# Kernel tuning notes

Measured on AMD Instinct MI355X. Metric: run time of the kernel, lower is better.

The kernel has to match this reference:

```python
import jax, jax.numpy as jnp
import numpy as np


def _l2norm(v, eps=1e-12):
    # torch F.normalize(dim=-1): v / clamp(||v||_2, min=eps)
    n = jnp.linalg.norm(v, axis=-1, keepdims=True)
    return v / jnp.maximum(n, eps)


def setup_inputs() -> dict:
    key = jax.random.key(0)
    ks = jax.random.split(key, 10)
    B, T, N, Ci, E, K, H = 64, 12, 1024, 64, 16, 3, 192
    O = H // 3  # subhidden size
    return {
        "x": jax.random.normal(ks[0], (B, N, Ci), jnp.float32),
        "x_window": jax.random.normal(ks[1], (B, T, N, 1), jnp.float32),
        "node_embeddings": jax.random.normal(ks[2], (N, E), jnp.float32) * 0.1,
        "ZPI": jax.random.normal(ks[3], (B, 3), jnp.float32),
        "supports_adj": jax.random.uniform(ks[4], (K, N, N), jnp.float32),
        "weights_pool": jax.random.normal(ks[5], (E, K, Ci, O), jnp.float32) * 0.1,
        "weights_pool_adj": jax.random.normal(ks[6], (E, K, Ci, O), jnp.float32) * 0.1,
        "weights_window": jax.random.normal(ks[7], (E, 1, O), jnp.float32) * 0.1,
        "bias_pool": jax.random.normal(ks[8], (E, H), jnp.float32) * 0.1,
        "T_param": jax.random.normal(ks[9], (T,), jnp.float32) * 0.1,
    }


def reference(x, x_window, node_embeddings, ZPI, supports_adj,
              weights_pool, weights_pool_adj, weights_window, bias_pool, T_param):
    N = node_embeddings.shape[0]
    K = weights_pool.shape[1]  # link_len

    # adaptive supports: softmax(relu(E E^T)) and its power series
    supports = jax.nn.softmax(jax.nn.relu(node_embeddings @ node_embeddings.T), axis=1)
    support_set = [jnp.eye(N, dtype=x.dtype), supports]
    for k in range(2, K):
        support_set.append(supports @ support_set[k - 1])
    S = jnp.stack(support_set, axis=0)  # (K, N, N)

    # per-node dynamic weights / bias
    weights = jnp.einsum('nd,dkio->nkio', node_embeddings, weights_pool)
    bias = node_embeddings @ bias_pool  # (N, H)

    # adaptive graph conv branch
    x_g = jnp.einsum('knm,bmc->bnkc', S, x)
    x_gconv = _l2norm(jnp.einsum('bnki,nkio->bno', x_g, weights))

    # static adjacency branch ('knn' repeated index = diagonal; sum over m --
    # faithful to the original torch einsum)
    weights_adj = jnp.einsum('nd,dkio->nkio', node_embeddings, weights_pool_adj)
    x_a = jnp.einsum('knn,bmc->bnkc', supports_adj, x)
    x_aconv = _l2norm(jnp.einsum('bnki,nkio->bno', x_a, weights_adj))

    # temporal window branch
    ww = jnp.einsum('nd,dio->nio', node_embeddings, weights_window)  # (N, 1, O)
    x_w = jnp.einsum('btni,nio->btno', x_window, ww)
    x_wconv = _l2norm(jnp.einsum('btno,t->bno', x_w, T_param))

    return jnp.concatenate([x_gconv, x_aconv, x_wconv], axis=-1) + bias
```

## Files before the change

kernel.cpp:

```cpp
#include <hip/hip_runtime.h>


typedef __attribute__((ext_vector_type(4))) float f32x4;
typedef __attribute__((ext_vector_type(8))) short short8;

#define DEVI static __device__ __forceinline__

DEVI short f2bf(float f) {
    unsigned int x = __builtin_bit_cast(unsigned int, f);
    x = (x + 0x7FFFu + ((x >> 16) & 1u)) >> 16;
    return (short)(unsigned short)x;
}
DEVI int swz(int row) { return ((row ^ (row >> 3)) & 7) << 3; }

DEVI f32x4 mfma16(short8 a, short8 b, f32x4 c) {
    return __builtin_amdgcn_mfma_f32_16x16x32_bf16(a, b, c, 0, 0, 0);
}

DEVI void gload16(const void* g, void* l) {
    __builtin_amdgcn_global_load_lds(
        (const __attribute__((address_space(1))) unsigned int*)g,
        (__attribute__((address_space(3))) unsigned int*)l, 16, 0, 0);
}

__global__ __launch_bounds__(256) void k_supports(const float* __restrict__ NE,
                                                  short* __restrict__ S) {
    int n = blockIdx.x, t = threadIdx.x;
    __shared__ float En[16];
    __shared__ float wsum[4];
    if (t < 16) En[t] = NE[n * 16 + t];
    __syncthreads();
    float e[4];
    float loc = 0.f;
#pragma unroll
    for (int i = 0; i < 4; ++i) {
        int m = t + 256 * i;
        const float* rp = NE + m * 16;
        float v = 0.f;
#pragma unroll
        for (int d = 0; d < 16; ++d) v += En[d] * rp[d];
        v = fmaxf(v, 0.f);
        e[i] = __expf(v);
        loc += e[i];
    }
#pragma unroll
    for (int off = 32; off; off >>= 1) loc += __shfl_xor(loc, off);
    if ((t & 63) == 0) wsum[t >> 6] = loc;
    __syncthreads();
    float inv = 1.f / (wsum[0] + wsum[1] + wsum[2] + wsum[3]);
#pragma unroll
    for (int i = 0; i < 4; ++i) S[n * 1024 + t + 256 * i] = f2bf(e[i] * inv);
}

__global__ __launch_bounds__(256) void k_small(
        const float* __restrict__ x, const float* __restrict__ xw,
        const float* __restrict__ NE, const float* __restrict__ adj,
        const float* __restrict__ wp, const float* __restrict__ wpa,
        const float* __restrict__ Tp,
        short* __restrict__ B2, short* __restrict__ A2,
        float* __restrict__ xsp, float* __restrict__ s_bn) {
    __shared__ float red[4][64];
    int bid = blockIdx.x, t = threadIdx.x;
    if (bid < 64) {
        int o = bid, j = t;
        short row[64];
        if (j < 192) {
            int kk = j >> 6, i = j & 63;
#pragma unroll
            for (int d = 0; d < 16; ++d)
                row[d] = f2bf(wp[((d * 3 + kk) * 64 + i) * 64 + o]);
#pragma unroll
            for (int k = 16; k < 64; ++k) row[k] = 0;
        } else {
            int i2 = j - 192;
#pragma unroll
            for (int k = 0; k < 16; ++k) row[k] = 0;
#pragma unroll
            for (int d = 0; d < 16; ++d)
#pragma unroll
                for (int kk = 0; kk < 3; ++kk)
                    row[16 + d * 3 + kk] = f2bf(wpa[((d * 3 + kk) * 64 + i2) * 64 + o]);
        }
        short* dst = B2 + (o * 256 + j) * 64;
#pragma unroll
        for (int q = 0; q < 8; ++q) {
            short8 v;
#pragma unroll
            for (int e2 = 0; e2 < 8; ++e2) v[e2] = row[q * 8 + e2];
            *reinterpret_cast<short8*>(dst + q * 8) = v;
        }
    } else if (bid < 320) {
        int idx = bid - 64, b = idx >> 2, mq = idx & 3;
        int c = t & 63, q2 = t >> 6;
        int m0 = mq * 256 + q2 * 64;
        float s = 0.f;
        for (int mm = 0; mm < 64; ++mm) s += x[(b * 1024 + m0 + mm) * 64 + c];
        red[q2][c] = s;
        __syncthreads();
        if (t < 64) xsp[(b * 4 + mq) * 64 + t] = red[0][t] + red[1][t] + red[2][t] + red[3][t];
    } else if (bid < 336) {
        int idx = bid - 320;
        float tp[12];
#pragma unroll
        for (int i = 0; i < 12; ++i) tp[i] = Tp[i];
        for (int bb = 0; bb < 4; ++bb) {
            int b = idx * 4 + bb;
#pragma unroll
            for (int j2 = 0; j2 < 4; ++j2) {
                int nn = t + 256 * j2;
                float s = 0.f;
#pragma unroll
                for (int tt = 0; tt < 12; ++tt) s += xw[(b * 12 + tt) * 1024 + nn] * tp[tt];
                s_bn[b * 1024 + nn] = s;
            }
        }
    } else {
        int n = (bid - 336) * 256 + t;
        float En[16];
#pragma unroll
        for (int d = 0; d < 16; ++d) En[d] = NE[n * 16 + d];
        float dg[3];
#pragma unroll
        for (int k = 0; k < 3; ++k) dg[k] = adj[k * 1024 * 1024 + n * 1024 + n];
        short row[64];
#pragma unroll
        for (int d = 0; d < 16; ++d) row[d] = f2bf(En[d]);
#pragma unroll
        for (int d = 0; d < 16; ++d)
#pragma unroll
            for (int k = 0; k < 3; ++k) row[16 + d * 3 + k] = f2bf(En[d] * dg[k]);
        short* dst = A2 + n * 64;
#pragma unroll
        for (int q = 0; q < 8; ++q) {
            short8 v;
#pragma unroll
            for (int e2 = 0; e2 < 8; ++e2) v[e2] = row[q * 8 + e2];
            *reinterpret_cast<short8*>(dst + q * 8) = v;
        }
    }
}

__global__ __launch_bounds__(256) void k_prep(const float* __restrict__ x,
                                              const short* __restrict__ S,
                                              const float* __restrict__ xsp,
                                              short* __restrict__ ST,
                                              short* __restrict__ XT,
                                              short* __restrict__ xs_bf) {
    __shared__ __align__(16) short Tbuf[64 * 128];
    int bid = blockIdx.x, t = threadIdx.x;
    if (bid < 512) {
        int b = bid >> 3, m0 = (bid & 7) * 128;
        const float* xp = x + ((size_t)b * 1024 + m0) * 64;
#pragma unroll
        for (int p = 0; p < 8; ++p) {
            int idx = t + 256 * p;
            int r = idx >> 4, c4 = (idx & 15) * 4;
            float4 v = *reinterpret_cast<const float4*>(&xp[r * 64 + c4]);
            Tbuf[(c4 + 0) * 128 + r] = f2bf(v.x);
            Tbuf[(c4 + 1) * 128 + r] = f2bf(v.y);
            Tbuf[(c4 + 2) * 128 + r] = f2bf(v.z);
            Tbuf[(c4 + 3) * 128 + r] = f2bf(v.w);
        }
        __syncthreads();
#pragma unroll
        for (int p = 0; p < 4; ++p) {
            int idx = t + 256 * p;
            int c = idx >> 4, q = idx & 15;
            *reinterpret_cast<short8*>(&XT[((size_t)b * 64 + c) * 1024 + m0 + q * 8]) =
                *reinterpret_cast<const short8*>(&Tbuf[c * 128 + q * 8]);
        }
    } else if (bid < 768) {
        int idx = bid - 512, bi = idx >> 4, bj = idx & 15;
        int c8 = (t & 7) * 8;
#pragma unroll
        for (int p = 0; p < 2; ++p) {
            int r = (t >> 3) + 32 * p;
            short8 v = *reinterpret_cast<const short8*>(
                &S[(size_t)(bi * 64 + r) * 1024 + bj * 64 + c8]);
#pragma unroll
            for (int e = 0; e < 8; ++e) Tbuf[(c8 + e) * 64 + r] = v[e];
        }
        __syncthreads();
#pragma unroll
        for (int p = 0; p < 2; ++p) {
            int r = (t >> 3) + 32 * p;
            *reinterpret_cast<short8*>(&ST[(size_t)(bj * 64 + r) * 1024 + bi * 64 + c8]) =
                *reinterpret_cast<const short8*>(&Tbuf[r * 64 + c8]);
        }
    } else {
        int j = (bid - 768) * 256 + t;
        int b = j >> 6, c = j & 63;
        float s = xsp[(b * 4 + 0) * 64 + c] + xsp[(b * 4 + 1) * 64 + c] +
                  xsp[(b * 4 + 2) * 64 + c] + xsp[(b * 4 + 3) * 64 + c];
        xs_bf[j] = f2bf(s);
    }
}

DEVI void mm_tile(const short* __restrict__ A, const short* __restrict__ Bt,
                  short* __restrict__ C, int ldC) {
    __shared__ __align__(16) short As[128 * 64];
    __shared__ __align__(16) short Bs[128 * 64];
    int t = threadIdx.x, wid = t >> 6, lane = t & 63;
    int rsub = lane >> 3, csub = (lane & 7) * 8;
    int wm = wid & 1, wn = wid >> 1;
    int lr = lane & 15, lg = lane >> 4;
    f32x4 acc[4][4] = {};
    for (int kt = 0; kt < 16; ++kt) {
#pragma unroll
        for (int q = 0; q < 4; ++q) {
            int row = q * 32 + wid * 8;
            gload16(A + (size_t)(row + rsub) * 1024 + kt * 64 + csub, As + row * 64);
            gload16(Bt + (size_t)(row + rsub) * 1024 + kt * 64 + csub, Bs + row * 64);
        }
        __syncthreads();
#pragma unroll
        for (int ks = 0; ks < 2; ++ks) {
            int kk = ks * 32 + lg * 8;
            short8 af[4], bfv[4];
#pragma unroll
            for (int i = 0; i < 4; ++i)
                af[i] = *reinterpret_cast<const short8*>(&As[(wm * 64 + i * 16 + lr) * 64 + kk]);
#pragma unroll
            for (int i = 0; i < 4; ++i)
                bfv[i] = *reinterpret_cast<const short8*>(&Bs[(wn * 64 + i * 16 + lr) * 64 + kk]);
#pragma unroll
            for (int mf = 0; mf < 4; ++mf)
#pragma unroll
                for (int nf = 0; nf < 4; ++nf)
                    acc[mf][nf] = mfma16(af[mf], bfv[nf], acc[mf][nf]);
        }
        __syncthreads();
    }
#pragma unroll
    for (int mf = 0; mf < 4; ++mf)
#pragma unroll
        for (int nf = 0; nf < 4; ++nf)
#pragma unroll
            for (int r = 0; r < 4; ++r) {
                int g = wm * 64 + mf * 16 + lg * 4 + r;
                int j = wn * 64 + nf * 16 + lr;
                C[(size_t)g * ldC + j] = f2bf(acc[mf][nf][r]);
            }
}

__global__ __launch_bounds__(256) void k_gemmS2(const short* __restrict__ S,
                                                const short* __restrict__ ST,
                                                short* __restrict__ S2) {
    int bx = blockIdx.x, by = blockIdx.y;
    mm_tile(S + (size_t)by * 128 * 1024, ST + (size_t)bx * 128 * 1024,
            S2 + (size_t)by * 128 * 1024 + bx * 128, 1024);
}

__global__ __launch_bounds__(256) void k_gemmY(const short* __restrict__ S,
                                               const short* __restrict__ S2,
                                               const short* __restrict__ XT,
                                               short* __restrict__ Y) {
    int bx = blockIdx.x, by = blockIdx.y;
    const short* A = (by < 8) ? (S + (size_t)by * 128 * 1024)
                              : (S2 + (size_t)(by - 8) * 128 * 1024);
    mm_tile(A, XT + (size_t)bx * 128 * 1024,
            Y + (size_t)by * 128 * 4096 + bx * 128, 4096);
}

__global__ __launch_bounds__(256) void k_gemm_w(const short* __restrict__ A2,
                                                const short* __restrict__ B2,
                                                short* __restrict__ Wall) {
    int bx = blockIdx.x, by = blockIdx.y;
    __shared__ __align__(16) short As[128 * 64];
    __shared__ __align__(16) short Bs[128 * 64];
    int t = threadIdx.x;
#pragma unroll
    for (int i = 0; i < 4; ++i) {
        int slot = t + 256 * i;
        int row = slot >> 3, k8 = slot & 7;
        int sw = swz(row);
        short8 va = *reinterpret_cast<const short8*>(A2 + (by * 128 + row) * 64 + k8 * 8);
        *reinterpret_cast<short8*>(&As[row * 64 + ((k8 * 8) ^ sw)]) = va;
        short8 vb = *reinterpret_cast<const short8*>(B2 + (bx * 128 + row) * 64 + k8 * 8);
        *reinterpret_cast<short8*>(&Bs[row * 64 + ((k8 * 8) ^ sw)]) = vb;
    }
    __syncthreads();
    int w = t >> 6, l = t & 63;
    int wm = w & 1, wn = w >> 1;
    int lr = l & 15, lg = l >> 4;
    f32x4 acc[4][4] = {};
#pragma unroll
    for (int ks = 0; ks < 2; ++ks) {
        int kk = ks * 32 + lg * 8;
        short8 af[4], bfr[4];
#pragma unroll
        for (int mf = 0; mf < 4; ++mf) {
            int row = wm * 64 + mf * 16 + lr;
            af[mf] = *reinterpret_cast<const short8*>(&As[row * 64 + (kk ^ swz(row))]);
        }
#pragma unroll
        for (int nf = 0; nf < 4; ++nf) {
            int row = wn * 64 + nf * 16 + lr;
            bfr[nf] = *reinterpret_cast<const short8*>(&Bs[row * 64 + (kk ^ swz(row))]);
        }
#pragma unroll
        for (int mf = 0; mf < 4; ++mf)
#pragma unroll
            for (int nf = 0; nf < 4; ++nf)
                acc[mf][nf] = mfma16(af[mf], bfr[nf], acc[mf][nf]);
    }
#pragma unroll
    for (int mf = 0; mf < 4; ++mf)
#pragma unroll
        for (int nf = 0; nf < 4; ++nf)
#pragma unroll
            for (int r = 0; r < 4; ++r) {
                int row = by * 128 + wm * 64 + mf * 16 + lg * 4 + r;
                int col = bx * 128 + wn * 64 + nf * 16 + lr;
                Wall[(size_t)row * 16384 + col] = f2bf(acc[mf][nf][r]);
            }
}

__global__ __launch_bounds__(256) void k_epi(
        const float* __restrict__ x, const short* __restrict__ Y,
        const short* __restrict__ xs_bf, const float* __restrict__ s_bn,
        const short* __restrict__ Wall, const float* __restrict__ NE,
        const float* __restrict__ bp, const float* __restrict__ wwin,
        float* __restrict__ out) {
    int n = blockIdx.x, t = threadIdx.x;
    __shared__ __align__(16) short Ylds[64 * 256];
    __shared__ float E_l[16];
    __shared__ float bias_l[192];
    __shared__ float ww_l[64];
    __shared__ float sq_l[2][2][64];
    __shared__ float wwn_l;
    if (t < 16) E_l[t] = NE[n * 16 + t];
    __syncthreads();
    if (t < 192) {
        float s = 0.f;
#pragma unroll
        for (int d = 0; d < 16; ++d) s += E_l[d] * bp[d * 192 + t];
        bias_l[t] = s;
    } else {
        int o = t - 192;
        float s = 0.f;
#pragma unroll
        for (int d = 0; d < 16; ++d) s += E_l[d] * wwin[d * 64 + o];
        ww_l[o] = s;
    }
    int w = t >> 6, l = t & 63;
    int wm = w & 1, wn = w >> 1;
    int lr = l & 15, lg = l >> 4;
    short8 wf[8][2];
#pragma unroll
    for (int ks = 0; ks < 8; ++ks)
#pragma unroll
        for (int nf = 0; nf < 2; ++nf) {
            int o = wn * 32 + nf * 16 + lr;
            int k = ks * 32 + lg * 8;
            wf[ks][nf] = *reinterpret_cast<const short8*>(Wall + ((size_t)n * 64 + o) * 256 + k);
        }
    const short* y1r = Y + (size_t)n * 4096;
    const short* y2r = Y + (size_t)(1024 + n) * 4096;
#pragma unroll
    for (int it = 0; it < 8; ++it) {
        int part = it >> 1;
        int b = (it & 1) * 32 + (t >> 3);
        int q = t & 7;
        short8 v;
        if (part == 0) {
            const float4* p = reinterpret_cast<const float4*>(&x[((size_t)b * 1024 + n) * 64 + q * 8]);
            float4 p0 = p[0], p1 = p[1];
            v[0] = f2bf(p0.x); v[1] = f2bf(p0.y); v[2] = f2bf(p0.z); v[3] = f2bf(p0.w);
            v[4] = f2bf(p1.x); v[5] = f2bf(p1.y); v[6] = f2bf(p1.z); v[7] = f2bf(p1.w);
        } else if (part == 1) {
            v = *reinterpret_cast<const short8*>(&y1r[b * 64 + q * 8]);
        } else if (part == 2) {
            v = *reinterpret_cast<const short8*>(&y2r[b * 64 + q * 8]);
        } else {
            v = *reinterpret_cast<const short8*>(&xs_bf[b * 64 + q * 8]);
        }
        *reinterpret_cast<short8*>(&Ylds[b * 256 + ((part * 64 + q * 8) ^ swz(b))]) = v;
    }
    __syncthreads();
    if (t < 64) {
        float v = ww_l[t];
        float s2 = v * v;
#pragma unroll
        for (int off = 32; off; off >>= 1) s2 += __shfl_xor(s2, off);
        if (t == 0) wwn_l = sqrtf(s2);
    }
    f32x4 accg[2][2] = {};
    f32x4 acca[2][2] = {};
#pragma unroll
    for (int ks = 0; ks < 8; ++ks) {
        short8 af[2];
#pragma unroll
        for (int mf = 0; mf < 2; ++mf) {
            int b = wm * 32 + mf * 16 + lr;
            int k = ks * 32 + lg * 8;
            af[mf] = *reinterpret_cast<const short8*>(&Ylds[b * 256 + (k ^ swz(b))]);
        }
#pragma unroll
        for (int mf = 0; mf < 2; ++mf)
#pragma unroll
            for (int nf = 0; nf < 2; ++nf) {
                if (ks < 6) accg[mf][nf] = mfma16(af[mf], wf[ks][nf], accg[mf][nf]);
                else        acca[mf][nf] = mfma16(af[mf], wf[ks][nf], acca[mf][nf]);
            }
    }
#pragma unroll
    for (int mf = 0; mf < 2; ++mf)
#pragma unroll
        for (int r = 0; r < 4; ++r) {
            float sg = accg[mf][0][r] * accg[mf][0][r] + accg[mf][1][r] * accg[mf][1][r];
            float sa = acca[mf][0][r] * acca[mf][0][r] + acca[mf][1][r] * acca[mf][1][r];
#pragma unroll
            for (int off = 1; off < 16; off <<= 1) {
                sg += __shfl_xor(sg, off);
                sa += __shfl_xor(sa, off);
            }
            if (lr == 0) {
                int b = wm * 32 + mf * 16 + lg * 4 + r;
                sq_l[0][wn][b] = sg;
                sq_l[1][wn][b] = sa;
            }
        }
    __syncthreads();
#pragma unroll
    for (int mf = 0; mf < 2; ++mf)
#pragma unroll
        for (int r = 0; r < 4; ++r) {
            int b = wm * 32 + mf * 16 + lg * 4 + r;
            float ig = 1.f / fmaxf(sqrtf(sq_l[0][0][b] + sq_l[0][1][b]), 1e-12f);
            float ia = 1.f / fmaxf(sqrtf(sq_l[1][0][b] + sq_l[1][1][b]), 1e-12f);
            float* po = out + ((size_t)b * 1024 + n) * 192;
#pragma unroll
            for (int nf = 0; nf < 2; ++nf) {
                int o = wn * 32 + nf * 16 + lr;
                po[o]      = accg[mf][nf][r] * ig + bias_l[o];
                po[64 + o] = acca[mf][nf][r] * ia + bias_l[64 + o];
            }
        }
    float wwn = wwn_l;
#pragma unroll
    for (int it = 0; it < 16; ++it) {
        int b = it * 4 + (t >> 6);
        int o = t & 63;
        float s = s_bn[b * 1024 + n];
        float pre = s * ww_l[o];
        float nrm = fabsf(s) * wwn;
        out[((size_t)b * 1024 + n) * 192 + 128 + o] = pre / fmaxf(nrm, 1e-12f) + bias_l[128 + o];
    }
}

extern "C" void kernel_launch(void* const* d_in, const int* in_sizes, int n_in,
                              void* d_out, int out_size, void* d_ws, size_t ws_size,
                              hipStream_t stream) {
    const float* x    = (const float*)d_in[0];
    const float* xw   = (const float*)d_in[1];
    const float* NE   = (const float*)d_in[2];
    const float* adj  = (const float*)d_in[4];
    const float* wp   = (const float*)d_in[5];
    const float* wpa  = (const float*)d_in[6];
    const float* wwin = (const float*)d_in[7];
    const float* bp   = (const float*)d_in[8];
    const float* Tp   = (const float*)d_in[9];
    float* out = (float*)d_out;

    char* ws = (char*)d_ws;
    const size_t OFF_S    = 0;
    const size_t OFF_ST   = 2097152;
    const size_t OFF_S2   = 4194304;
    const size_t OFF_XT   = 6291456;
    const size_t OFF_WALL = 0;
    const size_t OFF_Y    = 33554432;
    const size_t OFF_A2   = 50331648;
    const size_t OFF_B2   = 50462720;
    const size_t OFF_XSP  = 52559872;
    const size_t OFF_XSBF = 52625408;
    const size_t OFF_SBN  = 52633600;
    const size_t NEED     = 52895744;
    if (ws_size < NEED) return;

    short* S     = (short*)(ws + OFF_S);
    short* ST    = (short*)(ws + OFF_ST);
    short* S2    = (short*)(ws + OFF_S2);
    short* XT    = (short*)(ws + OFF_XT);
    short* Wall  = (short*)(ws + OFF_WALL);
    short* Y     = (short*)(ws + OFF_Y);
    short* A2    = (short*)(ws + OFF_A2);
    short* B2    = (short*)(ws + OFF_B2);
    float* xsp   = (float*)(ws + OFF_XSP);
    short* xs_bf = (short*)(ws + OFF_XSBF);
    float* s_bn  = (float*)(ws + OFF_SBN);

    k_supports<<<1024, 256, 0, stream>>>(NE, S);
    k_small<<<340, 256, 0, stream>>>(x, xw, NE, adj, wp, wpa, Tp, B2, A2, xsp, s_bn);
    k_prep<<<784, 256, 0, stream>>>(x, S, xsp, ST, XT, xs_bf);
    k_gemmS2<<<dim3(8, 8), 256, 0, stream>>>(S, ST, S2);
    k_gemmY<<<dim3(32, 16), 256, 0, stream>>>(S, S2, XT, Y);
    k_gemm_w<<<dim3(128, 8), 256, 0, stream>>>(A2, B2, Wall);
    k_epi<<<1024, 256, 0, stream>>>(x, Y, xs_bf, s_bn, Wall, NE, bp, wwin, out);
}
```

Baseline: 118.7 us.

## Restructure GEMM schedule, fuse column sums into transpose, and relayout Y/Wall for epilogue

Folds the per-batch column sum of x into the transpose kernel, where the data is already loaded, instead of re-reading x in a separate pass. The S·X GEMM now runs in the same launch as the S·S GEMM, and S2·X runs in a second launch that also finishes the xs reduction. Y and Wall are written in a k-interleaved layout so the epilogue can read MFMA fragments straight from global memory instead of staging them through LDS. The Tbuf row stride is padded to reduce LDS bank conflicts. The risks are more scattered stores in the GEMM epilogues and uncoalesced-looking fragment loads in k_epi.

```diff
diff --git a/kernel.cpp b/kernel.cpp
--- a/kernel.cpp
+++ b/kernel.cpp
@@ -53,13 +53,11 @@
 }
 
 __global__ __launch_bounds__(256) void k_small(
-        const float* __restrict__ x, const float* __restrict__ xw,
-        const float* __restrict__ NE, const float* __restrict__ adj,
-        const float* __restrict__ wp, const float* __restrict__ wpa,
-        const float* __restrict__ Tp,
+        const float* __restrict__ xw, const float* __restrict__ NE,
+        const float* __restrict__ adj, const float* __restrict__ wp,
+        const float* __restrict__ wpa, const float* __restrict__ Tp,
         short* __restrict__ B2, short* __restrict__ A2,
-        float* __restrict__ xsp, float* __restrict__ s_bn) {
-    __shared__ float red[4][64];
+        float* __restrict__ s_bn) {
     int bid = blockIdx.x, t = threadIdx.x;
     if (bid < 64) {
         int o = bid, j = t;
@@ -89,17 +87,8 @@
             for (int e2 = 0; e2 < 8; ++e2) v[e2] = row[q * 8 + e2];
             *reinterpret_cast<short8*>(dst + q * 8) = v;
         }
-    } else if (bid < 320) {
-        int idx = bid - 64, b = idx >> 2, mq = idx & 3;
-        int c = t & 63, q2 = t >> 6;
-        int m0 = mq * 256 + q2 * 64;
-        float s = 0.f;
-        for (int mm = 0; mm < 64; ++mm) s += x[(b * 1024 + m0 + mm) * 64 + c];
-        red[q2][c] = s;
-        __syncthreads();
-        if (t < 64) xsp[(b * 4 + mq) * 64 + t] = red[0][t] + red[1][t] + red[2][t] + red[3][t];
-    } else if (bid < 336) {
-        int idx = bid - 320;
+    } else if (bid < 80) {
+        int idx = bid - 64;
         float tp[12];
 #pragma unroll
         for (int i = 0; i < 12; ++i) tp[i] = Tp[i];
@@ -115,7 +104,7 @@
             }
         }
     } else {
-        int n = (bid - 336) * 256 + t;
+        int n = (bid - 80) * 256 + t;
         float En[16];
 #pragma unroll
         for (int d = 0; d < 16; ++d) En[d] = NE[n * 16 + d];
@@ -142,34 +131,46 @@
 
 __global__ __launch_bounds__(256) void k_prep(const float* __restrict__ x,
                                               const short* __restrict__ S,
-                                              const float* __restrict__ xsp,
                                               short* __restrict__ ST,
                                               short* __restrict__ XT,
-                                              short* __restrict__ xs_bf) {
-    __shared__ __align__(16) short Tbuf[64 * 128];
+                                              float* __restrict__ xsp2) {
+    __shared__ __align__(16) short Tbuf[64 * 136];
+    __shared__ float red[16][64];
     int bid = blockIdx.x, t = threadIdx.x;
     if (bid < 512) {
         int b = bid >> 3, m0 = (bid & 7) * 128;
         const float* xp = x + ((size_t)b * 1024 + m0) * 64;
+        float4 sum4 = {0.f, 0.f, 0.f, 0.f};
+        int c4 = (t & 15) * 4;
 #pragma unroll
         for (int p = 0; p < 8; ++p) {
             int idx = t + 256 * p;
-            int r = idx >> 4, c4 = (idx & 15) * 4;
+            int r = idx >> 4;
             float4 v = *reinterpret_cast<const float4*>(&xp[r * 64 + c4]);
-            Tbuf[(c4 + 0) * 128 + r] = f2bf(v.x);
-            Tbuf[(c4 + 1) * 128 + r] = f2bf(v.y);
-            Tbuf[(c4 + 2) * 128 + r] = f2bf(v.z);
-            Tbuf[(c4 + 3) * 128 + r] = f2bf(v.w);
-        }
+            Tbuf[(c4 + 0) * 136 + r] = f2bf(v.x);
+            Tbuf[(c4 + 1) * 136 + r] = f2bf(v.y);
+            Tbuf[(c4 + 2) * 136 + r] = f2bf(v.z);
+            Tbuf[(c4 + 3) * 136 + r] = f2bf(v.w);
+            sum4.x += v.x; sum4.y += v.y; sum4.z += v.z; sum4.w += v.w;
+        }
+        int g = t >> 4;
+        red[g][c4 + 0] = sum4.x; red[g][c4 + 1] = sum4.y;
+        red[g][c4 + 2] = sum4.z; red[g][c4 + 3] = sum4.w;
         __syncthreads();
 #pragma unroll
         for (int p = 0; p < 4; ++p) {
             int idx = t + 256 * p;
             int c = idx >> 4, q = idx & 15;
             *reinterpret_cast<short8*>(&XT[((size_t)b * 64 + c) * 1024 + m0 + q * 8]) =
-                *reinterpret_cast<const short8*>(&Tbuf[c * 128 + q * 8]);
-        }
-    } else if (bid < 768) {
+                *reinterpret_cast<const short8*>(&Tbuf[c * 136 + q * 8]);
+        }
+        if (t < 64) {
+            float tot = 0.f;
+#pragma unroll
+            for (int gg = 0; gg < 16; ++gg) tot += red[gg][t];
+            xsp2[((size_t)b * 8 + (bid & 7)) * 64 + t] = tot;
+        }
+    } else {
         int idx = bid - 512, bi = idx >> 4, bj = idx & 15;
         int c8 = (t & 7) * 8;
 #pragma unroll
@@ -187,19 +188,12 @@
             *reinterpret_cast<short8*>(&ST[(size_t)(bj * 64 + r) * 1024 + bi * 64 + c8]) =
                 *reinterpret_cast<const short8*>(&Tbuf[r * 64 + c8]);
         }
-    } else {
-        int j = (bid - 768) * 256 + t;
-        int b = j >> 6, c = j & 63;
-        float s = xsp[(b * 4 + 0) * 64 + c] + xsp[(b * 4 + 1) * 64 + c] +
-                  xsp[(b * 4 + 2) * 64 + c] + xsp[(b * 4 + 3) * 64 + c];
-        xs_bf[j] = f2bf(s);
-    }
-}
-
-DEVI void mm_tile(const short* __restrict__ A, const short* __restrict__ Bt,
-                  short* __restrict__ C, int ldC) {
-    __shared__ __align__(16) short As[128 * 64];
-    __shared__ __align__(16) short Bs[128 * 64];
+    }
+}
+
+template <int MODE>
+DEVI void mm_tile(short* As, short* Bs, const short* __restrict__ A,
+                  const short* __restrict__ Bt, short* __restrict__ Cb, int kofs) {
     int t = threadIdx.x, wid = t >> 6, lane = t & 63;
     int rsub = lane >> 3, csub = (lane & 7) * 8;
     int wm = wid & 1, wn = wid >> 1;
@@ -239,27 +233,54 @@
             for (int r = 0; r < 4; ++r) {
                 int g = wm * 64 + mf * 16 + lg * 4 + r;
                 int j = wn * 64 + nf * 16 + lr;
-                C[(size_t)g * ldC + j] = f2bf(acc[mf][nf][r]);
-            }
-}
-
-__global__ __launch_bounds__(256) void k_gemmS2(const short* __restrict__ S,
-                                                const short* __restrict__ ST,
-                                                short* __restrict__ S2) {
+                if (MODE == 0) {
+                    Cb[(size_t)g * 1024 + j] = f2bf(acc[mf][nf][r]);
+                } else {
+                    int c = j & 63, bloc = j >> 6;
+                    Cb[(size_t)g * 8192 + (size_t)((kofs + c) >> 3) * 512 + bloc * 8 + (c & 7)] =
+                        f2bf(acc[mf][nf][r]);
+                }
+            }
+}
+
+__global__ __launch_bounds__(256) void k_gemmA(const short* __restrict__ S,
+                                               const short* __restrict__ ST,
+                                               const short* __restrict__ XT,
+                                               short* __restrict__ YE,
+                                               short* __restrict__ S2) {
+    __shared__ __align__(16) short As[128 * 64];
+    __shared__ __align__(16) short Bs[128 * 64];
     int bx = blockIdx.x, by = blockIdx.y;
-    mm_tile(S + (size_t)by * 128 * 1024, ST + (size_t)bx * 128 * 1024,
-            S2 + (size_t)by * 128 * 1024 + bx * 128, 1024);
-}
-
-__global__ __launch_bounds__(256) void k_gemmY(const short* __restrict__ S,
-                                               const short* __restrict__ S2,
+    if (bx < 32)
+        mm_tile<1>(As, Bs, S + (size_t)by * 131072, XT + (size_t)bx * 131072,
+                   YE + (size_t)by * 128 * 8192 + bx * 16, 0);
+    else
+        mm_tile<0>(As, Bs, S + (size_t)by * 131072, ST + (size_t)(bx - 32) * 131072,
+                   S2 + (size_t)by * 128 * 1024 + (bx - 32) * 128, 0);
+}
+
+__global__ __launch_bounds__(256) void k_gemmB(const short* __restrict__ S2,
                                                const short* __restrict__ XT,
-                                               short* __restrict__ Y) {
-    int bx = blockIdx.x, by = blockIdx.y;
-    const short* A = (by < 8) ? (S + (size_t)by * 128 * 1024)
-                              : (S2 + (size_t)(by - 8) * 128 * 1024);
-    mm_tile(A, XT + (size_t)bx * 128 * 1024,
-            Y + (size_t)by * 128 * 4096 + bx * 128, 4096);
+                                               short* __restrict__ YE,
+                                               const float* __restrict__ xsp2,
+                                               short* __restrict__ xs_bf) {
+    __shared__ __align__(16) short As[128 * 64];
+    __shared__ __align__(16) short Bs[128 * 64];
+    int bx = blockIdx.x, by = blockIdx.y, t = threadIdx.x;
+    if (bx == 32) {
+#pragma unroll
+        for (int p = 0; p < 2; ++p) {
+            int j = by * 512 + p * 256 + t;
+            int b = j >> 6, c = j & 63;
+            float s = 0.f;
+#pragma unroll
+            for (int mt = 0; mt < 8; ++mt) s += xsp2[((size_t)b * 8 + mt) * 64 + c];
+            xs_bf[j] = f2bf(s);
+        }
+        return;
+    }
+    mm_tile<1>(As, Bs, S2 + (size_t)by * 131072, XT + (size_t)bx * 131072,
+               YE + (size_t)by * 128 * 8192 + bx * 16, 64);
 }
 
 __global__ __launch_bounds__(256) void k_gemm_w(const short* __restrict__ A2,
@@ -312,18 +333,20 @@
             for (int r = 0; r < 4; ++r) {
                 int row = by * 128 + wm * 64 + mf * 16 + lg * 4 + r;
                 int col = bx * 128 + wn * 64 + nf * 16 + lr;
-                Wall[(size_t)row * 16384 + col] = f2bf(acc[mf][nf][r]);
+                int o = col >> 8, j = col & 255;
+                Wall[(size_t)row * 16384 + (size_t)(j >> 3) * 512 + o * 8 + (j & 7)] =
+                    f2bf(acc[mf][nf][r]);
             }
 }
 
 __global__ __launch_bounds__(256) void k_epi(
-        const float* __restrict__ x, const short* __restrict__ Y,
+        const float* __restrict__ x, const short* __restrict__ YE,
         const short* __restrict__ xs_bf, const float* __restrict__ s_bn,
         const short* __restrict__ Wall, const float* __restrict__ NE,
         const float* __restrict__ bp, const float* __restrict__ wwin,
         float* __restrict__ out) {
     int n = blockIdx.x, t = threadIdx.x;
-    __shared__ __align__(16) short Ylds[64 * 256];
+    __shared__ __align__(16) short xst[64 * 64];
     __shared__ float E_l[16];
     __shared__ float bias_l[192];
     __shared__ float ww_l[64];
@@ -343,39 +366,12 @@
         for (int d = 0; d < 16; ++d) s += E_l[d] * wwin[d * 64 + o];
         ww_l[o] = s;
     }
-    int w = t >> 6, l = t & 63;
-    int wm = w & 1, wn = w >> 1;
-    int lr = l & 15, lg = l >> 4;
-    short8 wf[8][2];
-#pragma unroll
-    for (int ks = 0; ks < 8; ++ks)
-#pragma unroll
-        for (int nf = 0; nf < 2; ++nf) {
-            int o = wn * 32 + nf * 16 + lr;
-            int k = ks * 32 + lg * 8;
-            wf[ks][nf] = *reinterpret_cast<const short8*>(Wall + ((size_t)n * 64 + o) * 256 + k);
-        }
-    const short* y1r = Y + (size_t)n * 4096;
-    const short* y2r = Y + (size_t)(1024 + n) * 4096;
-#pragma unroll
-    for (int it = 0; it < 8; ++it) {
-        int part = it >> 1;
-        int b = (it & 1) * 32 + (t >> 3);
-        int q = t & 7;
-        short8 v;
-        if (part == 0) {
-            const float4* p = reinterpret_cast<const float4*>(&x[((size_t)b * 1024 + n) * 64 + q * 8]);
-            float4 p0 = p[0], p1 = p[1];
-            v[0] = f2bf(p0.x); v[1] = f2bf(p0.y); v[2] = f2bf(p0.z); v[3] = f2bf(p0.w);
-            v[4] = f2bf(p1.x); v[5] = f2bf(p1.y); v[6] = f2bf(p1.z); v[7] = f2bf(p1.w);
-        } else if (part == 1) {
-            v = *reinterpret_cast<const short8*>(&y1r[b * 64 + q * 8]);
-        } else if (part == 2) {
-            v = *reinterpret_cast<const short8*>(&y2r[b * 64 + q * 8]);
-        } else {
-            v = *reinterpret_cast<const short8*>(&xs_bf[b * 64 + q * 8]);
-        }
-        *reinterpret_cast<short8*>(&Ylds[b * 256 + ((part * 64 + q * 8) ^ swz(b))]) = v;
+#pragma unroll
+    for (int p = 0; p < 2; ++p) {
+        int idx = t + 256 * p;
+        int b = idx >> 3, q = idx & 7;
+        short8 v = *reinterpret_cast<const short8*>(&xs_bf[b * 64 + q * 8]);
+        *reinterpret_cast<short8*>(&xst[b * 64 + ((q * 8) ^ swz(b))]) = v;
     }
     __syncthreads();
     if (t < 64) {
@@ -385,6 +381,9 @@
         for (int off = 32; off; off >>= 1) s2 += __shfl_xor(s2, off);
         if (t == 0) wwn_l = sqrtf(s2);
     }
+    int w = t >> 6, l = t & 63;
+    int wm = w & 1, wn = w >> 1;
+    int lr = l & 15, lg = l >> 4;
     f32x4 accg[2][2] = {};
     f32x4 acca[2][2] = {};
 #pragma unroll
@@ -393,15 +392,36 @@
 #pragma unroll
         for (int mf = 0; mf < 2; ++mf) {
             int b = wm * 32 + mf * 16 + lr;
-            int k = ks * 32 + lg * 8;
-            af[mf] = *reinterpret_cast<const short8*>(&Ylds[b * 256 + (k ^ swz(b))]);
+            int k0 = ks * 32 + lg * 8;
+            if (ks < 2) {
+                const float4* p =
+                    reinterpret_cast<const float4*>(&x[((size_t)b * 1024 + n) * 64 + k0]);
+                float4 p0 = p[0], p1 = p[1];
+                short8 v;
+                v[0] = f2bf(p0.x); v[1] = f2bf(p0.y); v[2] = f2bf(p0.z); v[3] = f2bf(p0.w);
+                v[4] = f2bf(p1.x); v[5] = f2bf(p1.y); v[6] = f2bf(p1.z); v[7] = f2bf(p1.w);
+                af[mf] = v;
+            } else if (ks < 6) {
+                af[mf] = *reinterpret_cast<const short8*>(
+                    &YE[(size_t)n * 8192 + (size_t)((k0 - 64) >> 3) * 512 + b * 8]);
+            } else {
+                af[mf] = *reinterpret_cast<const short8*>(
+                    &xst[b * 64 + ((k0 - 192) ^ swz(b))]);
+            }
+        }
+        short8 wfk[2];
+#pragma unroll
+        for (int nf = 0; nf < 2; ++nf) {
+            int o = wn * 32 + nf * 16 + lr;
+            wfk[nf] = *reinterpret_cast<const short8*>(
+                &Wall[(size_t)n * 16384 + (size_t)(ks * 4 + lg) * 512 + o * 8]);
         }
 #pragma unroll
         for (int mf = 0; mf < 2; ++mf)
 #pragma unroll
             for (int nf = 0; nf < 2; ++nf) {
-                if (ks < 6) accg[mf][nf] = mfma16(af[mf], wf[ks][nf], accg[mf][nf]);
-                else        acca[mf][nf] = mfma16(af[mf], wf[ks][nf], acca[mf][nf]);
+                if (ks < 6) accg[mf][nf] = mfma16(af[mf], wfk[nf], accg[mf][nf]);
+                else        acca[mf][nf] = mfma16(af[mf], wfk[nf], acca[mf][nf]);
             }
     }
 #pragma unroll
@@ -464,37 +484,37 @@
     float* out = (float*)d_out;
 
     char* ws = (char*)d_ws;
-    const size_t OFF_S    = 0;
-    const size_t OFF_ST   = 2097152;
-    const size_t OFF_S2   = 4194304;
-    const size_t OFF_XT   = 6291456;
-    const size_t OFF_WALL = 0;
-    const size_t OFF_Y    = 33554432;
+    const size_t OFF_YE   = 0;
+    const size_t OFF_S    = 16777216;
+    const size_t OFF_ST   = 18874368;
+    const size_t OFF_S2   = 20971520;
+    const size_t OFF_XT   = 23068672;
+    const size_t OFF_WALL = 16777216;
     const size_t OFF_A2   = 50331648;
     const size_t OFF_B2   = 50462720;
-    const size_t OFF_XSP  = 52559872;
-    const size_t OFF_XSBF = 52625408;
-    const size_t OFF_SBN  = 52633600;
-    const size_t NEED     = 52895744;
+    const size_t OFF_XSP2 = 52559872;
+    const size_t OFF_XSBF = 52690944;
+    const size_t OFF_SBN  = 52699136;
+    const size_t NEED     = 52961280;
     if (ws_size < NEED) return;
 
+    short* YE    = (short*)(ws + OFF_YE);
     short* S     = (short*)(ws + OFF_S);
     short* ST    = (short*)(ws + OFF_ST);
     short* S2    = (short*)(ws + OFF_S2);
     short* XT    = (short*)(ws + OFF_XT);
     short* Wall  = (short*)(ws + OFF_WALL);
-    short* Y     = (short*)(ws + OFF_Y);
     short* A2    = (short*)(ws + OFF_A2);
     short* B2    = (short*)(ws + OFF_B2);
-    float* xsp   = (float*)(ws + OFF_XSP);
+    float* xsp2  = (float*)(ws + OFF_XSP2);
     short* xs_bf = (short*)(ws + OFF_XSBF);
     float* s_bn  = (float*)(ws + OFF_SBN);
 
     k_supports<<<1024, 256, 0, stream>>>(NE, S);
-    k_small<<<340, 256, 0, stream>>>(x, xw, NE, adj, wp, wpa, Tp, B2, A2, xsp, s_bn);
-    k_prep<<<784, 256, 0, stream>>>(x, S, xsp, ST, XT, xs_bf);
-    k_gemmS2<<<dim3(8, 8), 256, 0, stream>>>(S, ST, S2);
-    k_gemmY<<<dim3(32, 16), 256, 0, stream>>>(S, S2, XT, Y);
+    k_small<<<84, 256, 0, stream>>>(xw, NE, adj, wp, wpa, Tp, B2, A2, s_bn);
+    k_prep<<<768, 256, 0, stream>>>(x, S, ST, XT, xsp2);
+    k_gemmA<<<dim3(40, 8), 256, 0, stream>>>(S, ST, XT, YE, S2);
+    k_gemmB<<<dim3(33, 8), 256, 0, stream>>>(S2, XT, YE, xsp2, xs_bf);
     k_gemm_w<<<dim3(128, 8), 256, 0, stream>>>(A2, B2, Wall);
-    k_epi<<<1024, 256, 0, stream>>>(x, Y, xs_bf, s_bn, Wall, NE, bp, wwin, out);
-}
+    k_epi<<<1024, 256, 0, stream>>>(x, YE, xs_bf, s_bn, Wall, NE, bp, wwin, out);
+}
```

Result: slower. 138.3 us (+16.5%).

## Replace S² GEMM with chained S·(S·x) GEMMs reading x directly

Applied to the files above, without the earlier changes.

Computes S²x as S·(S·x) through two GEMM kernels that read x (converted to bf16 in-kernel) and the intermediate directly. This removes the 1024³ S² product, the transpose prep kernel and the ST/XT buffers. The Wall and Y layouts are changed so the epilogue reads its MFMA operands straight from global memory, without staging them in LDS. The epilogue is split into two batch halves, and the xs_bf reduction is folded into an extra k_gemm_w block. The trade-off is an extra dependent GEMM launch and strided scatter stores of the intermediate.

```diff
diff --git a/kernel.cpp b/kernel.cpp
--- a/kernel.cpp
+++ b/kernel.cpp
@@ -94,7 +94,7 @@
         int c = t & 63, q2 = t >> 6;
         int m0 = mq * 256 + q2 * 64;
         float s = 0.f;
-        for (int mm = 0; mm < 64; ++mm) s += x[(b * 1024 + m0 + mm) * 64 + c];
+        for (int mm = 0; mm < 64; ++mm) s += x[((size_t)b * 1024 + m0 + mm) * 64 + c];
         red[q2][c] = s;
         __syncthreads();
         if (t < 64) xsp[(b * 4 + mq) * 64 + t] = red[0][t] + red[1][t] + red[2][t] + red[3][t];
@@ -140,135 +140,152 @@
     }
 }
 
-__global__ __launch_bounds__(256) void k_prep(const float* __restrict__ x,
-                                              const short* __restrict__ S,
-                                              const float* __restrict__ xsp,
-                                              short* __restrict__ ST,
-                                              short* __restrict__ XT,
-                                              short* __restrict__ xs_bf) {
-    __shared__ __align__(16) short Tbuf[64 * 128];
-    int bid = blockIdx.x, t = threadIdx.x;
-    if (bid < 512) {
-        int b = bid >> 3, m0 = (bid & 7) * 128;
-        const float* xp = x + ((size_t)b * 1024 + m0) * 64;
-#pragma unroll
-        for (int p = 0; p < 8; ++p) {
-            int idx = t + 256 * p;
-            int r = idx >> 4, c4 = (idx & 15) * 4;
-            float4 v = *reinterpret_cast<const float4*>(&xp[r * 64 + c4]);
-            Tbuf[(c4 + 0) * 128 + r] = f2bf(v.x);
-            Tbuf[(c4 + 1) * 128 + r] = f2bf(v.y);
-            Tbuf[(c4 + 2) * 128 + r] = f2bf(v.z);
-            Tbuf[(c4 + 3) * 128 + r] = f2bf(v.w);
-        }
-        __syncthreads();
-#pragma unroll
-        for (int p = 0; p < 4; ++p) {
-            int idx = t + 256 * p;
-            int c = idx >> 4, q = idx & 15;
-            *reinterpret_cast<short8*>(&XT[((size_t)b * 64 + c) * 1024 + m0 + q * 8]) =
-                *reinterpret_cast<const short8*>(&Tbuf[c * 128 + q * 8]);
-        }
-    } else if (bid < 768) {
-        int idx = bid - 512, bi = idx >> 4, bj = idx & 15;
-        int c8 = (t & 7) * 8;
-#pragma unroll
-        for (int p = 0; p < 2; ++p) {
-            int r = (t >> 3) + 32 * p;
-            short8 v = *reinterpret_cast<const short8*>(
-                &S[(size_t)(bi * 64 + r) * 1024 + bj * 64 + c8]);
-#pragma unroll
-            for (int e = 0; e < 8; ++e) Tbuf[(c8 + e) * 64 + r] = v[e];
-        }
-        __syncthreads();
-#pragma unroll
-        for (int p = 0; p < 2; ++p) {
-            int r = (t >> 3) + 32 * p;
-            *reinterpret_cast<short8*>(&ST[(size_t)(bj * 64 + r) * 1024 + bi * 64 + c8]) =
-                *reinterpret_cast<const short8*>(&Tbuf[r * 64 + c8]);
-        }
-    } else {
-        int j = (bid - 768) * 256 + t;
-        int b = j >> 6, c = j & 63;
-        float s = xsp[(b * 4 + 0) * 64 + c] + xsp[(b * 4 + 1) * 64 + c] +
-                  xsp[(b * 4 + 2) * 64 + c] + xsp[(b * 4 + 3) * 64 + c];
-        xs_bf[j] = f2bf(s);
-    }
-}
-
-DEVI void mm_tile(const short* __restrict__ A, const short* __restrict__ Bt,
-                  short* __restrict__ C, int ldC) {
+__global__ __launch_bounds__(256) void k_gemm1(const short* __restrict__ S,
+                                               const float* __restrict__ x,
+                                               short* __restrict__ YE) {
     __shared__ __align__(16) short As[128 * 64];
-    __shared__ __align__(16) short Bs[128 * 64];
-    int t = threadIdx.x, wid = t >> 6, lane = t & 63;
+    __shared__ __align__(16) short Bs[64 * 64];
+    int bx = blockIdx.x, b = blockIdx.y, t = threadIdx.x;
+    int wid = t >> 6, lane = t & 63;
     int rsub = lane >> 3, csub = (lane & 7) * 8;
     int wm = wid & 1, wn = wid >> 1;
     int lr = lane & 15, lg = lane >> 4;
-    f32x4 acc[4][4] = {};
+    const short* A = S + (size_t)bx * 131072;
+    const float* xb = x + (size_t)b * 65536;
+    int bm = t >> 2, bc = (t & 3) * 16;
+    f32x4 acc[4][2] = {};
     for (int kt = 0; kt < 16; ++kt) {
 #pragma unroll
         for (int q = 0; q < 4; ++q) {
             int row = q * 32 + wid * 8;
             gload16(A + (size_t)(row + rsub) * 1024 + kt * 64 + csub, As + row * 64);
-            gload16(Bt + (size_t)(row + rsub) * 1024 + kt * 64 + csub, Bs + row * 64);
+        }
+#pragma unroll
+        for (int j = 0; j < 4; ++j) {
+            float4 f = *reinterpret_cast<const float4*>(&xb[(kt * 64 + bm) * 64 + bc + 4 * j]);
+            float vv[4] = {f.x, f.y, f.z, f.w};
+#pragma unroll
+            for (int e = 0; e < 4; ++e) {
+                int c = bc + 4 * j + e;
+                Bs[c * 64 + (bm ^ swz(c))] = f2bf(vv[e]);
+            }
         }
         __syncthreads();
 #pragma unroll
         for (int ks = 0; ks < 2; ++ks) {
             int kk = ks * 32 + lg * 8;
-            short8 af[4], bfv[4];
+            short8 af[4], bfr[2];
 #pragma unroll
             for (int i = 0; i < 4; ++i)
                 af[i] = *reinterpret_cast<const short8*>(&As[(wm * 64 + i * 16 + lr) * 64 + kk]);
 #pragma unroll
+            for (int nf = 0; nf < 2; ++nf) {
+                int c = wn * 32 + nf * 16 + lr;
+                bfr[nf] = *reinterpret_cast<const short8*>(&Bs[c * 64 + (kk ^ swz(c))]);
+            }
+#pragma unroll
             for (int i = 0; i < 4; ++i)
-                bfv[i] = *reinterpret_cast<const short8*>(&Bs[(wn * 64 + i * 16 + lr) * 64 + kk]);
-#pragma unroll
-            for (int mf = 0; mf < 4; ++mf)
-#pragma unroll
-                for (int nf = 0; nf < 4; ++nf)
-                    acc[mf][nf] = mfma16(af[mf], bfv[nf], acc[mf][nf]);
+#pragma unroll
+                for (int nf = 0; nf < 2; ++nf)
+                    acc[i][nf] = mfma16(af[i], bfr[nf], acc[i][nf]);
         }
         __syncthreads();
     }
 #pragma unroll
-    for (int mf = 0; mf < 4; ++mf)
-#pragma unroll
-        for (int nf = 0; nf < 4; ++nf)
+    for (int i = 0; i < 4; ++i)
+#pragma unroll
+        for (int nf = 0; nf < 2; ++nf)
 #pragma unroll
             for (int r = 0; r < 4; ++r) {
-                int g = wm * 64 + mf * 16 + lg * 4 + r;
-                int j = wn * 64 + nf * 16 + lr;
-                C[(size_t)g * ldC + j] = f2bf(acc[mf][nf][r]);
-            }
-}
-
-__global__ __launch_bounds__(256) void k_gemmS2(const short* __restrict__ S,
-                                                const short* __restrict__ ST,
-                                                short* __restrict__ S2) {
-    int bx = blockIdx.x, by = blockIdx.y;
-    mm_tile(S + (size_t)by * 128 * 1024, ST + (size_t)bx * 128 * 1024,
-            S2 + (size_t)by * 128 * 1024 + bx * 128, 1024);
-}
-
-__global__ __launch_bounds__(256) void k_gemmY(const short* __restrict__ S,
-                                               const short* __restrict__ S2,
-                                               const short* __restrict__ XT,
-                                               short* __restrict__ Y) {
-    int bx = blockIdx.x, by = blockIdx.y;
-    const short* A = (by < 8) ? (S + (size_t)by * 128 * 1024)
-                              : (S2 + (size_t)(by - 8) * 128 * 1024);
-    mm_tile(A, XT + (size_t)bx * 128 * 1024,
-            Y + (size_t)by * 128 * 4096 + bx * 128, 4096);
+                int g = wm * 64 + i * 16 + lg * 4 + r;
+                int c = wn * 32 + nf * 16 + lr;
+                YE[(size_t)(bx * 128 + g) * 8192 + (size_t)(c >> 3) * 512 + b * 8 + (c & 7)] =
+                    f2bf(acc[i][nf][r]);
+            }
+}
+
+__global__ __launch_bounds__(256) void k_gemm2(const short* __restrict__ S,
+                                               const short* __restrict__ YEin,
+                                               short* __restrict__ YE) {
+    __shared__ __align__(16) short As[128 * 64];
+    __shared__ __align__(16) short Bs[64 * 64];
+    int bx = blockIdx.x, b = blockIdx.y, t = threadIdx.x;
+    int wid = t >> 6, lane = t & 63;
+    int rsub = lane >> 3, csub = (lane & 7) * 8;
+    int wm = wid & 1, wn = wid >> 1;
+    int lr = lane & 15, lg = lane >> 4;
+    const short* A = S + (size_t)bx * 131072;
+    int bm = t >> 2, q0 = (t & 3) * 2;
+    f32x4 acc[4][2] = {};
+    for (int kt = 0; kt < 16; ++kt) {
+#pragma unroll
+        for (int q = 0; q < 4; ++q) {
+            int row = q * 32 + wid * 8;
+            gload16(A + (size_t)(row + rsub) * 1024 + kt * 64 + csub, As + row * 64);
+        }
+#pragma unroll
+        for (int j = 0; j < 2; ++j) {
+            short8 v = *reinterpret_cast<const short8*>(
+                &YEin[(size_t)(kt * 64 + bm) * 8192 + (size_t)(q0 + j) * 512 + b * 8]);
+#pragma unroll
+            for (int e = 0; e < 8; ++e) {
+                int c = (q0 + j) * 8 + e;
+                Bs[c * 64 + (bm ^ swz(c))] = v[e];
+            }
+        }
+        __syncthreads();
+#pragma unroll
+        for (int ks = 0; ks < 2; ++ks) {
+            int kk = ks * 32 + lg * 8;
+            short8 af[4], bfr[2];
+#pragma unroll
+            for (int i = 0; i < 4; ++i)
+                af[i] = *reinterpret_cast<const short8*>(&As[(wm * 64 + i * 16 + lr) * 64 + kk]);
+#pragma unroll
+            for (int nf = 0; nf < 2; ++nf) {
+                int c = wn * 32 + nf * 16 + lr;
+                bfr[nf] = *reinterpret_cast<const short8*>(&Bs[c * 64 + (kk ^ swz(c))]);
+            }
+#pragma unroll
+            for (int i = 0; i < 4; ++i)
+#pragma unroll
+                for (int nf = 0; nf < 2; ++nf)
+                    acc[i][nf] = mfma16(af[i], bfr[nf], acc[i][nf]);
+        }
+        __syncthreads();
+    }
+#pragma unroll
+    for (int i = 0; i < 4; ++i)
+#pragma unroll
+        for (int nf = 0; nf < 2; ++nf)
+#pragma unroll
+            for (int r = 0; r < 4; ++r) {
+                int g = wm * 64 + i * 16 + lg * 4 + r;
+                int c = wn * 32 + nf * 16 + lr;
+                YE[(size_t)(bx * 128 + g) * 8192 + (size_t)(8 + (c >> 3)) * 512 + b * 8 + (c & 7)] =
+                    f2bf(acc[i][nf][r]);
+            }
 }
 
 __global__ __launch_bounds__(256) void k_gemm_w(const short* __restrict__ A2,
                                                 const short* __restrict__ B2,
-                                                short* __restrict__ Wall) {
-    int bx = blockIdx.x, by = blockIdx.y;
+                                                short* __restrict__ Wall,
+                                                const float* __restrict__ xsp,
+                                                short* __restrict__ xs_bf) {
+    int bx = blockIdx.x, by = blockIdx.y, t = threadIdx.x;
+    if (bx == 128) {
+#pragma unroll
+        for (int p = 0; p < 2; ++p) {
+            int j = by * 512 + p * 256 + t;
+            int b = j >> 6, c = j & 63;
+            float s = xsp[(b * 4 + 0) * 64 + c] + xsp[(b * 4 + 1) * 64 + c] +
+                      xsp[(b * 4 + 2) * 64 + c] + xsp[(b * 4 + 3) * 64 + c];
+            xs_bf[j] = f2bf(s);
+        }
+        return;
+    }
     __shared__ __align__(16) short As[128 * 64];
     __shared__ __align__(16) short Bs[128 * 64];
-    int t = threadIdx.x;
 #pragma unroll
     for (int i = 0; i < 4; ++i) {
         int slot = t + 256 * i;
@@ -312,22 +329,24 @@
             for (int r = 0; r < 4; ++r) {
                 int row = by * 128 + wm * 64 + mf * 16 + lg * 4 + r;
                 int col = bx * 128 + wn * 64 + nf * 16 + lr;
-                Wall[(size_t)row * 16384 + col] = f2bf(acc[mf][nf][r]);
+                int o = col >> 8, j = col & 255;
+                Wall[(size_t)row * 16384 + (size_t)(j >> 3) * 512 + o * 8 + (j & 7)] =
+                    f2bf(acc[mf][nf][r]);
             }
 }
 
 __global__ __launch_bounds__(256) void k_epi(
-        const float* __restrict__ x, const short* __restrict__ Y,
+        const float* __restrict__ x, const short* __restrict__ YE,
         const short* __restrict__ xs_bf, const float* __restrict__ s_bn,
         const short* __restrict__ Wall, const float* __restrict__ NE,
         const float* __restrict__ bp, const float* __restrict__ wwin,
         float* __restrict__ out) {
-    int n = blockIdx.x, t = threadIdx.x;
-    __shared__ __align__(16) short Ylds[64 * 256];
+    int n = blockIdx.x, bh = blockIdx.y, t = threadIdx.x;
+    __shared__ __align__(16) short xst[32 * 64];
     __shared__ float E_l[16];
     __shared__ float bias_l[192];
     __shared__ float ww_l[64];
-    __shared__ float sq_l[2][2][64];
+    __shared__ float sq_l[2][2][32];
     __shared__ float wwn_l;
     if (t < 16) E_l[t] = NE[n * 16 + t];
     __syncthreads();
@@ -343,105 +362,91 @@
         for (int d = 0; d < 16; ++d) s += E_l[d] * wwin[d * 64 + o];
         ww_l[o] = s;
     }
+    {
+        int bl = t >> 3, q = t & 7;
+        short8 v = *reinterpret_cast<const short8*>(&xs_bf[(bh * 32 + bl) * 64 + q * 8]);
+        *reinterpret_cast<short8*>(&xst[bl * 64 + ((q * 8) ^ swz(bl))]) = v;
+    }
+    __syncthreads();
+    if (t < 64) {
+        float v = ww_l[t];
+        float s2 = v * v;
+#pragma unroll
+        for (int off = 32; off; off >>= 1) s2 += __shfl_xor(s2, off);
+        if (t == 0) wwn_l = sqrtf(s2);
+    }
     int w = t >> 6, l = t & 63;
     int wm = w & 1, wn = w >> 1;
     int lr = l & 15, lg = l >> 4;
-    short8 wf[8][2];
-#pragma unroll
-    for (int ks = 0; ks < 8; ++ks)
+    f32x4 accg[2] = {};
+    f32x4 acca[2] = {};
+#pragma unroll
+    for (int ks = 0; ks < 8; ++ks) {
+        int k0 = ks * 32 + lg * 8;
+        int bl = wm * 16 + lr;
+        int b = bh * 32 + bl;
+        short8 af;
+        if (ks < 2) {
+            const float4* p = reinterpret_cast<const float4*>(&x[((size_t)b * 1024 + n) * 64 + k0]);
+            float4 p0 = p[0], p1 = p[1];
+            short8 v;
+            v[0] = f2bf(p0.x); v[1] = f2bf(p0.y); v[2] = f2bf(p0.z); v[3] = f2bf(p0.w);
+            v[4] = f2bf(p1.x); v[5] = f2bf(p1.y); v[6] = f2bf(p1.z); v[7] = f2bf(p1.w);
+            af = v;
+        } else if (ks < 6) {
+            af = *reinterpret_cast<const short8*>(
+                &YE[(size_t)n * 8192 + (size_t)((k0 - 64) >> 3) * 512 + b * 8]);
+        } else {
+            af = *reinterpret_cast<const short8*>(&xst[bl * 64 + ((k0 - 192) ^ swz(bl))]);
+        }
+        short8 wfk[2];
 #pragma unroll
         for (int nf = 0; nf < 2; ++nf) {
             int o = wn * 32 + nf * 16 + lr;
-            int k = ks * 32 + lg * 8;
-            wf[ks][nf] = *reinterpret_cast<const short8*>(Wall + ((size_t)n * 64 + o) * 256 + k);
-        }
-    const short* y1r = Y + (size_t)n * 4096;
-    const short* y2r = Y + (size_t)(1024 + n) * 4096;
+            wfk[nf] = *reinterpret_cast<const short8*>(
+                &Wall[(size_t)n * 16384 + (size_t)(ks * 4 + lg) * 512 + o * 8]);
+        }
+#pragma unroll
+        for (int nf = 0; nf < 2; ++nf) {
+            if (ks < 6) accg[nf] = mfma16(af, wfk[nf], accg[nf]);
+            else        acca[nf] = mfma16(af, wfk[nf], acca[nf]);
+        }
+    }
+#pragma unroll
+    for (int r = 0; r < 4; ++r) {
+        float sg = accg[0][r] * accg[0][r] + accg[1][r] * accg[1][r];
+        float sa = acca[0][r] * acca[0][r] + acca[1][r] * acca[1][r];
+#pragma unroll
+        for (int off = 1; off < 16; off <<= 1) {
+            sg += __shfl_xor(sg, off);
+            sa += __shfl_xor(sa, off);
+        }
+        if (lr == 0) {
+            int bl = wm * 16 + lg * 4 + r;
+            sq_l[0][wn][bl] = sg;
+            sq_l[1][wn][bl] = sa;
+        }
+    }
+    __syncthreads();
+#pragma unroll
+    for (int r = 0; r < 4; ++r) {
+        int bl = wm * 16 + lg * 4 + r;
+        float ig = 1.f / fmaxf(sqrtf(sq_l[0][0][bl] + sq_l[0][1][bl]), 1e-12f);
+        float ia = 1.f / fmaxf(sqrtf(sq_l[1][0][bl] + sq_l[1][1][bl]), 1e-12f);
+        float* po = out + (((size_t)bh * 32 + bl) * 1024 + n) * 192;
+#pragma unroll
+        for (int nf = 0; nf < 2; ++nf) {
+            int o = wn * 32 + nf * 16 + lr;
+            po[o]      = accg[nf][r] * ig + bias_l[o];
+            po[64 + o] = acca[nf][r] * ia + bias_l[64 + o];
+        }
+    }
+    float wwn = wwn_l;
 #pragma unroll
     for (int it = 0; it < 8; ++it) {
-        int part = it >> 1;
-        int b = (it & 1) * 32 + (t >> 3);
-        int q = t & 7;
-        short8 v;
-        if (part == 0) {
-            const float4* p = reinterpret_cast<const float4*>(&x[((size_t)b * 1024 + n) * 64 + q * 8]);
-            float4 p0 = p[0], p1 = p[1];
-            v[0] = f2bf(p0.x); v[1] = f2bf(p0.y); v[2] = f2bf(p0.z); v[3] = f2bf(p0.w);
-            v[4] = f2bf(p1.x); v[5] = f2bf(p1.y); v[6] = f2bf(p1.z); v[7] = f2bf(p1.w);
-        } else if (part == 1) {
-            v = *reinterpret_cast<const short8*>(&y1r[b * 64 + q * 8]);
-        } else if (part == 2) {
-            v = *reinterpret_cast<const short8*>(&y2r[b * 64 + q * 8]);
-        } else {
-            v = *reinterpret_cast<const short8*>(&xs_bf[b * 64 + q * 8]);
-        }
-        *reinterpret_cast<short8*>(&Ylds[b * 256 + ((part * 64 + q * 8) ^ swz(b))]) = v;
-    }
-    __syncthreads();
-    if (t < 64) {
-        float v = ww_l[t];
-        float s2 = v * v;
-#pragma unroll
-        for (int off = 32; off; off >>= 1) s2 += __shfl_xor(s2, off);
-        if (t == 0) wwn_l = sqrtf(s2);
-    }
-    f32x4 accg[2][2] = {};
-    f32x4 acca[2][2] = {};
-#pragma unroll
-    for (int ks = 0; ks < 8; ++ks) {
-        short8 af[2];
-#pragma unroll
-        for (int mf = 0; mf < 2; ++mf) {
-            int b = wm * 32 + mf * 16 + lr;
-            int k = ks * 32 + lg * 8;
-            af[mf] = *reinterpret_cast<const short8*>(&Ylds[b * 256 + (k ^ swz(b))]);
-        }
-#pragma unroll
-        for (int mf = 0; mf < 2; ++mf)
-#pragma unroll
-            for (int nf = 0; nf < 2; ++nf) {
-                if (ks < 6) accg[mf][nf] = mfma16(af[mf], wf[ks][nf], accg[mf][nf]);
-                else        acca[mf][nf] = mfma16(af[mf], wf[ks][nf], acca[mf][nf]);
-            }
-    }
-#pragma unroll
-    for (int mf = 0; mf < 2; ++mf)
-#pragma unroll
-        for (int r = 0; r < 4; ++r) {
-            float sg = accg[mf][0][r] * accg[mf][0][r] + accg[mf][1][r] * accg[mf][1][r];
-            float sa = acca[mf][0][r] * acca[mf][0][r] + acca[mf][1][r] * acca[mf][1][r];
-#pragma unroll
-            for (int off = 1; off < 16; off <<= 1) {
-                sg += __shfl_xor(sg, off);
-                sa += __shfl_xor(sa, off);
-            }
-            if (lr == 0) {
-                int b = wm * 32 + mf * 16 + lg * 4 + r;
-                sq_l[0][wn][b] = sg;
-                sq_l[1][wn][b] = sa;
-            }
-        }
-    __syncthreads();
-#pragma unroll
-    for (int mf = 0; mf < 2; ++mf)
-#pragma unroll
-        for (int r = 0; r < 4; ++r) {
-            int b = wm * 32 + mf * 16 + lg * 4 + r;
-            float ig = 1.f / fmaxf(sqrtf(sq_l[0][0][b] + sq_l[0][1][b]), 1e-12f);
-            float ia = 1.f / fmaxf(sqrtf(sq_l[1][0][b] + sq_l[1][1][b]), 1e-12f);
-            float* po = out + ((size_t)b * 1024 + n) * 192;
-#pragma unroll
-            for (int nf = 0; nf < 2; ++nf) {
-                int o = wn * 32 + nf * 16 + lr;
-                po[o]      = accg[mf][nf][r] * ig + bias_l[o];
-                po[64 + o] = acca[mf][nf][r] * ia + bias_l[64 + o];
-            }
-        }
-    float wwn = wwn_l;
-#pragma unroll
-    for (int it = 0; it < 16; ++it) {
-        int b = it * 4 + (t >> 6);
+        int bl = it * 4 + (t >> 6);
         int o = t & 63;
+        int b = bh * 32 + bl;
         float s = s_bn[b * 1024 + n];
         float pre = s * ww_l[o];
         float nrm = fabsf(s) * wwn;
@@ -465,25 +470,19 @@
 
     char* ws = (char*)d_ws;
     const size_t OFF_S    = 0;
-    const size_t OFF_ST   = 2097152;
-    const size_t OFF_S2   = 4194304;
-    const size_t OFF_XT   = 6291456;
-    const size_t OFF_WALL = 0;
-    const size_t OFF_Y    = 33554432;
-    const size_t OFF_A2   = 50331648;
-    const size_t OFF_B2   = 50462720;
-    const size_t OFF_XSP  = 52559872;
-    const size_t OFF_XSBF = 52625408;
-    const size_t OFF_SBN  = 52633600;
-    const size_t NEED     = 52895744;
+    const size_t OFF_YE   = 2097152;
+    const size_t OFF_WALL = 18874368;
+    const size_t OFF_A2   = 52428800;
+    const size_t OFF_B2   = 52559872;
+    const size_t OFF_XSP  = 54657024;
+    const size_t OFF_XSBF = 54722560;
+    const size_t OFF_SBN  = 54730752;
+    const size_t NEED     = 54992896;
     if (ws_size < NEED) return;
 
     short* S     = (short*)(ws + OFF_S);
-    short* ST    = (short*)(ws + OFF_ST);
-    short* S2    = (short*)(ws + OFF_S2);
-    short* XT    = (short*)(ws + OFF_XT);
+    short* YE    = (short*)(ws + OFF_YE);
     short* Wall  = (short*)(ws + OFF_WALL);
-    short* Y     = (short*)(ws + OFF_Y);
     short* A2    = (short*)(ws + OFF_A2);
     short* B2    = (short*)(ws + OFF_B2);
     float* xsp   = (float*)(ws + OFF_XSP);
@@ -492,9 +491,8 @@
 
     k_supports<<<1024, 256, 0, stream>>>(NE, S);
     k_small<<<340, 256, 0, stream>>>(x, xw, NE, adj, wp, wpa, Tp, B2, A2, xsp, s_bn);
-    k_prep<<<784, 256, 0, stream>>>(x, S, xsp, ST, XT, xs_bf);
-    k_gemmS2<<<dim3(8, 8), 256, 0, stream>>>(S, ST, S2);
-    k_gemmY<<<dim3(32, 16), 256, 0, stream>>>(S, S2, XT, Y);
-    k_gemm_w<<<dim3(128, 8), 256, 0, stream>>>(A2, B2, Wall);
-    k_epi<<<1024, 256, 0, stream>>>(x, Y, xs_bf, s_bn, Wall, NE, bp, wwin, out);
-}
+    k_gemm1<<<dim3(8, 64), 256, 0, stream>>>(S, x, YE);
+    k_gemm2<<<dim3(8, 64), 256, 0, stream>>>(S, YE, YE);
+    k_gemm_w<<<dim3(129, 8), 256, 0, stream>>>(A2, B2, Wall, xsp, xs_bf);
+    k_epi<<<dim3(1024, 2), 256, 0, stream>>>(x, YE, xs_bf, s_bn, Wall, NE, bp, wwin, out);
+}
```

Result: slower. 135.7 us (+14.4%).
